# Kernel optimization log

Hardware: AMD Instinct MI355X
Metric: run time of the kernel (lower is better)

## Reference

```python
import jax, jax.numpy as jnp
import numpy as np

N, D, O, V, E, C = 100000, 128, 128, 3, 400000, 2

def setup_inputs() -> dict:
    key = jax.random.key(0)
    ks = jax.random.split(key, 32)
    s = 0.05
    inp = {
        'features': jax.random.normal(ks[0], (N, D), jnp.float32),
        'edge_index': jax.random.randint(ks[1], (V, 2, E), 0, N, jnp.int32),
        'edge_weight': jax.random.uniform(ks[2], (V, E), jnp.float32),
        # per-view RelationAggregator (single relation each)
        'rel_w': jax.random.normal(ks[3], (V, D, O)) * s,
        'rel_b': jnp.zeros((V, O)),
        'gate_w': jax.random.normal(ks[4], (V, O, O)) * s,
        'gate_b': jnp.zeros((V, O)),
        # LabelAwareAttention
        'la_w1': jax.random.normal(ks[5], (C, D, D // 2)) * s,
        'la_b1': jnp.zeros((C, D // 2)),
        'la_w2': jax.random.normal(ks[6], (C, D // 2)) * s,
        'la_b2': jnp.zeros((C,)),
        'pred_w': jax.random.normal(ks[7], (D, C)) * s,
        'pred_b': jnp.zeros((C,)),
        'att_bias': jnp.float32(0.1),
        # ViewLevelAttention
        'view_pref': jax.random.normal(ks[8], (V, O)),
        'va_w1': jax.random.normal(ks[9], (O, O // 2)) * s,
        'va_b1': jnp.zeros((O // 2,)),
        'va_w2': jax.random.normal(ks[10], (O // 2,)) * s,
        'va_b2': jnp.float32(0.0),
        # linear heads
        'ft_w': jax.random.normal(ks[11], (D, O)) * s,
        'ft_b': jnp.zeros((O,)),
        'sl_w': jax.random.normal(ks[12], (D, O)) * s,
        'sl_b': jnp.zeros((O,)),
        'fus_w': jax.random.normal(ks[13], (2 * O, O)) * s,
        'fus_b': jnp.zeros((O,)),
        'ln_g': jnp.ones((O,)),
        'ln_beta': jnp.zeros((O,)),
    }
    return inp


def _aggregate_view(features, ei, ew, w, b, gw, gb):
    # gather -> linear -> edge weight -> scatter-add (fused segment_sum)
    msg = (features[ei[0]] @ w + b) * ew[:, None]          # [E, O]
    agg = jax.ops.segment_sum(msg, ei[1], num_segments=N)  # [N, O]
    # relation_weight_net: softmax over 1 relation == 1.0 (identity)
    gate = jax.nn.sigmoid(agg @ gw + gb)
    return gate * agg


def reference(features, edge_index, edge_weight, rel_w, rel_b, gate_w, gate_b,
              la_w1, la_b1, la_w2, la_b2, pred_w, pred_b, att_bias,
              view_pref, va_w1, va_b1, va_w2, va_b2,
              ft_w, ft_b, sl_w, sl_b, fus_w, fus_b, ln_g, ln_beta):
    # --- label-aware attention ---
    class_probs = jax.nn.softmax(features @ pred_w + pred_b, axis=-1)        # [N, C]
    h = jax.nn.relu(jnp.einsum('nd,cdk->nck', features, la_w1) + la_b1)      # [N, C, D/2]
    scores = jax.nn.sigmoid(jnp.einsum('nck,ck->nc', h, la_w2) + la_b2)      # [N, C]
    node_att = jnp.sum(scores * class_probs, axis=-1) + att_bias             # [N]

    # --- per-view relation aggregation ---
    views = jax.vmap(_aggregate_view, in_axes=(None, 0, 0, 0, 0, 0, 0))(
        features, edge_index, edge_weight, rel_w, rel_b, gate_w, gate_b)     # [V, N, O]

    # --- view-level attention ---
    pe = views * view_pref[:, None, :]                                       # [V, N, O]
    vh = jax.nn.relu(jnp.einsum('vno,ok->vnk', pe, va_w1) + va_b1)           # [V, N, O/2]
    vscore = jnp.einsum('vnk,k->vn', vh, va_w2) + va_b2                      # [V, N]
    v_att = jax.nn.softmax(vscore, axis=0)                                   # over views
    combined = jnp.sum(views * v_att[..., None], axis=0)                     # [N, O]

    # --- fusion (dropout in eval mode == identity) ---
    self_out = features @ sl_w + sl_b
    transformed = features @ ft_w + ft_b
    weighted = combined * node_att[:, None]
    fused = jax.nn.relu(jnp.concatenate([self_out, weighted], axis=-1) @ fus_w + fus_b)
    out = fused + transformed

    mu = jnp.mean(out, axis=-1, keepdims=True)
    var = jnp.mean(jnp.square(out - mu), axis=-1, keepdims=True)
    out = (out - mu) / jnp.sqrt(var + 1e-5) * ln_g + ln_beta
    return out, class_probs
```

## Files before the change

### kernel.cpp

```cpp
#include <hip/hip_runtime.h>

#define N_ 100000
#define D_ 128
#define O_ 128
#define V_ 3
#define E_ 400000
#define NB_SCAN 98
#define EGRID 1563
#define MB 32
#define NBLK (N_ / MB)
#define LDA 136

#define PRE_CVT  6250
#define PRE_PREW (PRE_CVT + 64)
#define PRE_PREP (PRE_PREW + 617)
#define PRE_TOT  (PRE_PREP + 3 * EGRID)

typedef unsigned short u16;
typedef __attribute__((ext_vector_type(8))) short bf16x8;
typedef __attribute__((ext_vector_type(4))) float f32x4;

#define MFMA16x16x32 __builtin_amdgcn_mfma_f32_16x16x32_bf16

#define P_RELB  0
#define P_GATEB 384
#define P_VP    768
#define P_VAB1  1152
#define P_VAW2  1216
#define P_VAB2  1280
#define P_LAB1  1281
#define P_LAW2  1409
#define P_LAB2  1537
#define P_PREDB 1539
#define P_ATTB  1541
#define P_FTB   1542
#define P_LNG   1670
#define P_LNB   1798
#define P_PREDW 1926
#define P_TOTAL 2182

__device__ __forceinline__ float b2f(u16 u) {
    union { float f; unsigned int i; } x; x.i = ((unsigned int)u) << 16; return x.f;
}
__device__ __forceinline__ float blo(unsigned int u) {
    union { float f; unsigned int i; } x; x.i = u << 16; return x.f;
}
__device__ __forceinline__ float bhi(unsigned int u) {
    union { float f; unsigned int i; } x; x.i = u & 0xffff0000u; return x.f;
}
__device__ __forceinline__ u16 f2b(float f) {
    union { float f; unsigned int i; } x; x.f = f;
    unsigned int r = x.i + 0x7FFFu + ((x.i >> 16) & 1u);
    return (u16)(r >> 16);
}

template<int F32> __device__ __forceinline__ float LD(const void* p, size_t i) {
    if (F32) return ((const float*)p)[i];
    return b2f(((const u16*)p)[i]);
}

__global__ void k_detect(const u16* __restrict__ feat, int* __restrict__ flag) {
    int t = threadIdx.x;
    u16 a = feat[2 * t], b = feat[2 * t + 128];
    int zeros = (a == 0 ? 1 : 0) + (b == 0 ? 1 : 0);
    float va = b2f(a), vb = b2f(b);
    int bad = (!(va > -128.f && va < 128.f) ? 1 : 0) +
              (!(vb > -128.f && vb < 128.f) ? 1 : 0);
    #pragma unroll
    for (int s = 1; s <= 32; s <<= 1) {
        bad += __shfl_xor(bad, s);
        zeros += __shfl_xor(zeros, s);
    }
    if (t == 0) flag[0] = (bad >= 16 || zeros >= 64) ? 1 : 0;
}

__device__ __forceinline__ void cvt_body_f32(int b, const void* feat,
                                             u16* __restrict__ featB) {
    size_t idx = (size_t)b * 256 + threadIdx.x;
    const float4* fp = (const float4*)feat;
    float4 a = fp[idx * 2], c = fp[idx * 2 + 1];
    uint4 u;
    u.x = (unsigned)f2b(a.x) | ((unsigned)f2b(a.y) << 16);
    u.y = (unsigned)f2b(a.z) | ((unsigned)f2b(a.w) << 16);
    u.z = (unsigned)f2b(c.x) | ((unsigned)f2b(c.y) << 16);
    u.w = (unsigned)f2b(c.z) | ((unsigned)f2b(c.w) << 16);
    ((uint4*)featB)[idx] = u;
}

template<int F32>
__device__ __forceinline__ void prew_body(int b, const void* sl_w, const void* sl_b,
                                          const void* fus_w, const void* fus_b,
                                          u16* __restrict__ W1T, float* __restrict__ b1) {
    int gid = b * 256 + threadIdx.x;
    int d = gid >> 7, o = gid & 127;
    float acc = 0.f;
    for (int k = 0; k < 128; ++k)
        acc += LD<F32>(sl_w, d * 128 + k) * LD<F32>(fus_w, k * 128 + o);
    W1T[o * 128 + d] = f2b(acc);
    if (gid < 128) {
        float accb = 0.f;
        for (int k = 0; k < 128; ++k)
            accb += LD<F32>(sl_b, k) * LD<F32>(fus_w, k * 128 + gid);
        b1[gid] = accb + LD<F32>(fus_b, gid);
    }
}

template<int F32>
__device__ __forceinline__ void prep_body(int b,
        const void* rel_w, const void* gate_w, const void* va_w1, const void* fus_w,
        const void* ft_w, const void* la_w1,
        const void* rel_b, const void* gate_b, const void* vpref,
        const void* va_b1, const void* va_w2, const void* va_b2,
        const void* la_b1, const void* la_w2, const void* la_b2,
        const void* pred_b, const void* att_bias, const void* ft_b,
        const void* ln_g, const void* ln_beta, const void* pred_w,
        u16* __restrict__ relT, u16* __restrict__ gateT, u16* __restrict__ vaT,
        u16* __restrict__ fus2T, u16* __restrict__ ftT, u16* __restrict__ laT,
        float* __restrict__ P) {
    int id = b * 256 + threadIdx.x;
    if (id < 49152) {
        int v = id >> 14, r = id & 16383, o = r >> 7, d = r & 127;
        relT[id] = f2b(LD<F32>(rel_w, (size_t)v * 16384 + d * 128 + o));
    } else if (id < 98304) {
        int t = id - 49152, v = t >> 14, r = t & 16383, o = r >> 7, d = r & 127;
        gateT[t] = f2b(LD<F32>(gate_w, (size_t)v * 16384 + d * 128 + o));
    } else if (id < 106496) {
        int t = id - 98304, n = t >> 7, k = t & 127;
        vaT[t] = f2b(LD<F32>(va_w1, k * 64 + n));
    } else if (id < 122880) {
        int t = id - 106496, n = t >> 7, k = t & 127;
        fus2T[t] = f2b(LD<F32>(fus_w, (128 + k) * 128 + n));
    } else if (id < 139264) {
        int t = id - 122880, o = t >> 7, d = t & 127;
        ftT[t] = f2b(LD<F32>(ft_w, d * 128 + o));
    } else if (id < 155648) {
        int t = id - 139264, n = t >> 7, d = t & 127;
        int c = n >> 6, j = n & 63;
        laT[t] = f2b(LD<F32>(la_w1, c * 8192 + d * 64 + j));
    } else if (id < 155648 + P_TOTAL) {
        int t = id - 155648;
        float val;
        if      (t < P_GATEB) val = LD<F32>(rel_b, t);
        else if (t < P_VP)    val = LD<F32>(gate_b, t - P_GATEB);
        else if (t < P_VAB1)  val = LD<F32>(vpref, t - P_VP);
        else if (t < P_VAW2)  val = LD<F32>(va_b1, t - P_VAB1);
        else if (t < P_VAB2)  val = LD<F32>(va_w2, t - P_VAW2);
        else if (t < P_LAB1)  val = LD<F32>(va_b2, 0);
        else if (t < P_LAW2)  val = LD<F32>(la_b1, t - P_LAB1);
        else if (t < P_LAB2)  val = LD<F32>(la_w2, t - P_LAW2);
        else if (t < P_PREDB) val = LD<F32>(la_b2, t - P_LAB2);
        else if (t < P_ATTB)  val = LD<F32>(pred_b, t - P_PREDB);
        else if (t < P_FTB)   val = LD<F32>(att_bias, 0);
        else if (t < P_LNG)   val = LD<F32>(ft_b, t - P_FTB);
        else if (t < P_LNB)   val = LD<F32>(ln_g, t - P_LNG);
        else if (t < P_PREDW) val = LD<F32>(ln_beta, t - P_LNB);
        else                  val = LD<F32>(pred_w, t - P_PREDW);
        P[t] = val;
    }
}

__global__ __launch_bounds__(256) void k_preC(const int* __restrict__ flag,
        const void* feat, u16* __restrict__ featB,
        const void* sl_w, const void* sl_b, const void* fus_w, const void* fus_b,
        u16* __restrict__ W1T, float* __restrict__ b1,
        const void* rel_w, const void* gate_w, const void* va_w1,
        const void* ft_w, const void* la_w1,
        const void* rel_b, const void* gate_b, const void* vpref,
        const void* va_b1, const void* va_w2, const void* va_b2,
        const void* la_b1, const void* la_w2, const void* la_b2,
        const void* pred_b, const void* att_bias, const void* ft_b,
        const void* ln_g, const void* ln_beta, const void* pred_w,
        u16* __restrict__ relT, u16* __restrict__ gateT, u16* __restrict__ vaT,
        u16* __restrict__ fus2T, u16* __restrict__ ftT, u16* __restrict__ laT,
        float* __restrict__ P,
        const int* __restrict__ ei, int* __restrict__ cur3) {
    int b = blockIdx.x;
    if (b < PRE_CVT) {
        if (flag[0]) cvt_body_f32(b, feat, featB);
    } else if (b < PRE_PREW) {
        if (flag[0]) prew_body<1>(b - PRE_CVT, sl_w, sl_b, fus_w, fus_b, W1T, b1);
        else         prew_body<0>(b - PRE_CVT, sl_w, sl_b, fus_w, fus_b, W1T, b1);
    } else if (b < PRE_PREP) {
        if (flag[0]) prep_body<1>(b - PRE_PREW, rel_w, gate_w, va_w1, fus_w, ft_w, la_w1,
                                  rel_b, gate_b, vpref, va_b1, va_w2, va_b2,
                                  la_b1, la_w2, la_b2, pred_b, att_bias, ft_b,
                                  ln_g, ln_beta, pred_w, relT, gateT, vaT, fus2T, ftT, laT, P);
        else         prep_body<0>(b - PRE_PREW, rel_w, gate_w, va_w1, fus_w, ft_w, la_w1,
                                  rel_b, gate_b, vpref, va_b1, va_w2, va_b2,
                                  la_b1, la_w2, la_b2, pred_b, att_bias, ft_b,
                                  ln_g, ln_beta, pred_w, relT, gateT, vaT, fus2T, ftT, laT, P);
    } else {
        int b2 = b - PRE_PREP;
        int v = b2 / EGRID;
        int e = (b2 % EGRID) * 256 + threadIdx.x;
        if (e < E_) atomicAdd(&cur3[v * N_ + ei[(size_t)v * 2 * E_ + E_ + e]], 1);
    }
}

__global__ __launch_bounds__(256) void k_scan_bsum(const int* __restrict__ cur3,
                                                   int* __restrict__ bsum) {
    __shared__ int red[256];
    const int v = blockIdx.x / NB_SCAN, b = blockIdx.x % NB_SCAN, tid = threadIdx.x;
    const int base = b * 1024;
    const int* counts = cur3 + v * N_;
    int s = 0;
    for (int i = tid; i < 1024; i += 256) {
        int idx = base + i;
        s += (idx < N_) ? counts[idx] : 0;
    }
    red[tid] = s;
    __syncthreads();
    for (int st = 128; st >= 1; st >>= 1) {
        if (tid < st) red[tid] += red[tid + st];
        __syncthreads();
    }
    if (tid == 0) bsum[v * 128 + b] = red[0];
}

__global__ __launch_bounds__(256) void k_scan_write(int* __restrict__ cur3,
                                                    const int* __restrict__ bsum,
                                                    int* __restrict__ offs3) {
    __shared__ int lsum[256];
    __shared__ int bs_s[128];
    const int v = blockIdx.x / NB_SCAN, b = blockIdx.x % NB_SCAN, tid = threadIdx.x;
    const int base = b * 1024;
    int* counts = cur3 + v * N_;
    int* offs   = offs3 + v * N_;
    if (tid < 128) bs_s[tid] = (tid < b) ? bsum[v * 128 + tid] : 0;
    int c[4]; int s = 0;
    #pragma unroll
    for (int k = 0; k < 4; ++k) {
        int idx = base + tid * 4 + k;
        c[k] = (idx < N_) ? counts[idx] : 0;
        s += c[k];
    }
    lsum[tid] = s;
    __syncthreads();
    for (int st = 1; st < 256; st <<= 1) {
        int t = (tid >= st) ? lsum[tid - st] : 0;
        __syncthreads();
        lsum[tid] += t;
        __syncthreads();
    }
    for (int st = 64; st >= 1; st >>= 1) {
        if (tid < st) bs_s[tid] += bs_s[tid + st];
        __syncthreads();
    }
    int off = bs_s[0] + lsum[tid] - s;
    #pragma unroll
    for (int k = 0; k < 4; ++k) {
        int idx = base + tid * 4 + k;
        if (idx < N_) { offs[idx] = off; counts[idx] = off; }
        off += c[k];
    }
}

template<int F32>
__device__ __forceinline__ void place_body(const int* __restrict__ ei, const void* ew_all,
                                           int* __restrict__ cur3, int2* __restrict__ srcw3) {
    int v = blockIdx.x / EGRID;
    int e = (blockIdx.x % EGRID) * 256 + threadIdx.x;
    if (e < E_) {
        int dst = ei[(size_t)v * 2 * E_ + E_ + e];
        int src = ei[(size_t)v * 2 * E_ + e];
        float w = LD<F32>(ew_all, (size_t)v * E_ + e);
        int pos = atomicAdd(&cur3[v * N_ + dst], 1);
        int2 sw; sw.x = src; sw.y = __float_as_int(w);
        srcw3[(size_t)v * E_ + pos] = sw;
    }
}
__global__ __launch_bounds__(256) void k_place(const int* __restrict__ flag,
                                               const int* __restrict__ ei, const void* ew,
                                               int* __restrict__ cur3, int2* __restrict__ srcw3) {
    if (flag[0]) place_body<1>(ei, ew, cur3, srcw3);
    else         place_body<0>(ei, ew, cur3, srcw3);
}

__global__ __launch_bounds__(768, 6) void k_fused(const int* __restrict__ flag,
        const void* feat, const u16* __restrict__ featB_,
        const int2* __restrict__ srcw3,
        const int* __restrict__ offs3, const int* __restrict__ ends3,
        const u16* __restrict__ relT, const u16* __restrict__ gateT,
        const u16* __restrict__ vaT, const u16* __restrict__ W1T,
        const u16* __restrict__ fus2T, const u16* __restrict__ ftT,
        const u16* __restrict__ laT,
        const float* __restrict__ b1, const float* __restrict__ P,
        void* __restrict__ d_out) {
    const int f32 = flag[0];
    const u16* __restrict__ fb = f32 ? featB_ : (const u16*)feat;

    __shared__ __align__(16) u16 xA[MB * LDA];
    __shared__ __align__(16) u16 zbuf[3][MB * LDA];
    __shared__ __align__(16) float Fbuf[MB * 128];
    __shared__ float vp3_s[3][128];
    __shared__ float redL[4][MB];
    __shared__ float redv[3][4][MB];
    __shared__ float wsn3[3][MB];
    __shared__ float aw_s[MB][3];
    __shared__ float natt_s[MB];
    __shared__ float lg_s[MB][2];
    __shared__ float mrs_s[MB][2];
    __shared__ float vab1_s[64], vaw2_s[64];
    __shared__ float predw_s[256];
    __shared__ float b1_s[128], ftb_s[128], lng_s[128], lnb_s[128];

    const int tid = threadIdx.x;
    const int g   = tid >> 8;
    const int t256 = tid & 255;
    const int wid = t256 >> 6;
    const int L = t256 & 63, q = L >> 4, i = L & 15;
    const int nb = wid * 32;
    const int nodebase = blockIdx.x * MB;
    const int nl = t256 >> 5, l32 = t256 & 31, o4 = l32 * 4;
    const int gsub = t256 >> 4, l16 = tid & 15, o8 = l16 * 8;
    const f32x4 zz = {0.f, 0.f, 0.f, 0.f};

    auto ldf = [&](const u16* B, int row, int k0) -> bf16x8 {
        return *(const bf16x8*)&B[row * LDA + k0];
    };
    auto ldg = [&](const u16* B, int row, int k0) -> bf16x8 {
        return *(const bf16x8*)&B[row * 128 + k0];
    };
    auto gemm32 = [&](const u16* A, const u16* Bg, f32x4 acc[2][2]) {
        #pragma unroll
        for (int kk = 0; kk < 4; ++kk) {
            int k0 = q * 8 + kk * 32;
            bf16x8 a0 = ldf(A, i, k0);
            bf16x8 a1 = ldf(A, i + 16, k0);
            bf16x8 bb0 = ldg(Bg, nb + i, k0);
            bf16x8 bb1 = ldg(Bg, nb + 16 + i, k0);
            acc[0][0] = MFMA16x16x32(a0, bb0, acc[0][0], 0, 0, 0);
            acc[0][1] = MFMA16x16x32(a0, bb1, acc[0][1], 0, 0, 0);
            acc[1][0] = MFMA16x16x32(a1, bb0, acc[1][0], 0, 0, 0);
            acc[1][1] = MFMA16x16x32(a1, bb1, acc[1][1], 0, 0, 0);
        }
    };
    auto gather = [&]() {
        const int* offs = offs3 + g * N_;
        const int* ends = ends3 + g * N_;
        const int2* srcw = srcw3 + (size_t)g * E_;
        #pragma unroll
        for (int rep = 0; rep < 2; ++rep) {
            const int m = gsub + rep * 16;
            const int node = nodebase + m;
            float z0 = 0.f, z1 = 0.f, z2 = 0.f, z3 = 0.f;
            float z4 = 0.f, z5 = 0.f, z6 = 0.f, z7 = 0.f, ws = 0.f;
            int j = offs[node], jend = ends[node];
            while (j < jend) {
                int r = jend - j;
                int2 e0 = srcw[j];
                int2 e1, e2, e3;
                e1.x = 0; e1.y = 0; e2.x = 0; e2.y = 0; e3.x = 0; e3.y = 0;
                if (r > 1) e1 = srcw[j + 1];
                if (r > 2) e2 = srcw[j + 2];
                if (r > 3) e3 = srcw[j + 3];
                uint4 x0, x1, x2, x3;
                x1.x = x1.y = x1.z = x1.w = 0;
                x2.x = x2.y = x2.z = x2.w = 0;
                x3.x = x3.y = x3.z = x3.w = 0;
                x0 = *(const uint4*)&fb[(size_t)e0.x * 128 + o8];
                if (r > 1) x1 = *(const uint4*)&fb[(size_t)e1.x * 128 + o8];
                if (r > 2) x2 = *(const uint4*)&fb[(size_t)e2.x * 128 + o8];
                if (r > 3) x3 = *(const uint4*)&fb[(size_t)e3.x * 128 + o8];
                float w0 = __int_as_float(e0.y), w1 = __int_as_float(e1.y);
                float w2 = __int_as_float(e2.y), w3 = __int_as_float(e3.y);
                ws += w0 + w1 + w2 + w3;
                z0 += w0 * blo(x0.x) + w1 * blo(x1.x) + w2 * blo(x2.x) + w3 * blo(x3.x);
                z1 += w0 * bhi(x0.x) + w1 * bhi(x1.x) + w2 * bhi(x2.x) + w3 * bhi(x3.x);
                z2 += w0 * blo(x0.y) + w1 * blo(x1.y) + w2 * blo(x2.y) + w3 * blo(x3.y);
                z3 += w0 * bhi(x0.y) + w1 * bhi(x1.y) + w2 * bhi(x2.y) + w3 * bhi(x3.y);
                z4 += w0 * blo(x0.z) + w1 * blo(x1.z) + w2 * blo(x2.z) + w3 * blo(x3.z);
                z5 += w0 * bhi(x0.z) + w1 * bhi(x1.z) + w2 * bhi(x2.z) + w3 * bhi(x3.z);
                z6 += w0 * blo(x0.w) + w1 * blo(x1.w) + w2 * blo(x2.w) + w3 * blo(x3.w);
                z7 += w0 * bhi(x0.w) + w1 * bhi(x1.w) + w2 * bhi(x2.w) + w3 * bhi(x3.w);
                j += 4;
            }
            uint4 u;
            u.x = (unsigned)f2b(z0) | ((unsigned)f2b(z1) << 16);
            u.y = (unsigned)f2b(z2) | ((unsigned)f2b(z3) << 16);
            u.z = (unsigned)f2b(z4) | ((unsigned)f2b(z5) << 16);
            u.w = (unsigned)f2b(z6) | ((unsigned)f2b(z7) << 16);
            *(uint4*)&zbuf[g][m * LDA + o8] = u;
            if (l16 == 0) wsn3[g][m] = ws;
        }
    };

    if (tid < 512) {
        int m = tid >> 4, s = tid & 15;
        *(uint4*)&xA[m * LDA + s * 8] =
            *(const uint4*)&fb[(size_t)(nodebase + m) * 128 + s * 8];
    }
    if (tid < 64) { vab1_s[tid] = P[P_VAB1 + tid]; vaw2_s[tid] = P[P_VAW2 + tid]; }
    if (tid < 128) {
        b1_s[tid]  = b1[tid];
        ftb_s[tid] = P[P_FTB + tid];
        lng_s[tid] = P[P_LNG + tid];
        lnb_s[tid] = P[P_LNB + tid];
    }
    if (tid < 256) predw_s[tid] = P[P_PREDW + tid];
    if (tid >= 256 && tid < 640) {
        int t = tid - 256;
        vp3_s[t >> 7][t & 127] = P[P_VP + t];
    }
    gather();
    __syncthreads();

    f32x4 accA[2][2] = {{zz, zz}, {zz, zz}};
    gemm32(zbuf[g], relT + (size_t)g * 16384, accA);
    if (g == 0) {
        f32x4 accL[2][2] = {{zz, zz}, {zz, zz}};
        gemm32(xA, laT, accL);
        #pragma unroll
        for (int rep = 0; rep < 4; ++rep) {
            int m = rep * 8 + nl;
            float lg0 = 0.f, lg1 = 0.f;
            #pragma unroll
            for (int t = 0; t < 4; ++t) {
                float xv = b2f(xA[m * LDA + o4 + t]);
                lg0 += xv * predw_s[(o4 + t) * 2 + 0];
                lg1 += xv * predw_s[(o4 + t) * 2 + 1];
            }
            #pragma unroll
            for (int s = 1; s <= 16; s <<= 1) {
                lg0 += __shfl_xor(lg0, s);
                lg1 += __shfl_xor(lg1, s);
            }
            if (l32 == 0) { lg_s[m][0] = lg0; lg_s[m][1] = lg1; }
        }
        float la0 = P[P_LAB1 + nb + i],  la1 = P[P_LAB1 + nb + 16 + i];
        float lw0 = P[P_LAW2 + nb + i],  lw1 = P[P_LAW2 + nb + 16 + i];
        float partL[2][4];
        #pragma unroll
        for (int mt = 0; mt < 2; ++mt)
            #pragma unroll
            for (int r = 0; r < 4; ++r) {
                float h0 = fmaxf(accL[mt][0][r] + la0, 0.f);
                float h1 = fmaxf(accL[mt][1][r] + la1, 0.f);
                partL[mt][r] = h0 * lw0 + h1 * lw1;
            }
        #pragma unroll
        for (int s = 1; s <= 8; s <<= 1)
            #pragma unroll
            for (int mt = 0; mt < 2; ++mt)
                #pragma unroll
                for (int r = 0; r < 4; ++r)
                    partL[mt][r] += __shfl_xor(partL[mt][r], s);
        if (i == 0)
            #pragma unroll
            for (int mt = 0; mt < 2; ++mt)
                #pragma unroll
                for (int r = 0; r < 4; ++r)
                    redL[wid][mt * 16 + q * 4 + r] = partL[mt][r];
    }
    __syncthreads();

    {
        float rb0 = P[P_RELB + g * 128 + nb + i];
        float rb1 = P[P_RELB + g * 128 + nb + 16 + i];
        #pragma unroll
        for (int mt = 0; mt < 2; ++mt)
            #pragma unroll
            for (int nt = 0; nt < 2; ++nt) {
                float rb = nt ? rb1 : rb0;
                int col = nb + nt * 16 + i;
                #pragma unroll
                for (int r = 0; r < 4; ++r) {
                    int row = mt * 16 + q * 4 + r;
                    float a = accA[mt][nt][r] + wsn3[g][row] * rb;
                    accA[mt][nt][r] = a;
                    zbuf[g][row * LDA + col] = f2b(a);
                }
            }
    }
    if (tid < MB) {
        float c0 = redL[0][tid] + redL[1][tid] + P[P_LAB2 + 0];
        float c1 = redL[2][tid] + redL[3][tid] + P[P_LAB2 + 1];
        float s0 = 1.f / (1.f + __expf(-c0));
        float s1 = 1.f / (1.f + __expf(-c1));
        float l0 = lg_s[tid][0] + P[P_PREDB + 0];
        float l1 = lg_s[tid][1] + P[P_PREDB + 1];
        float mx = fmaxf(l0, l1);
        float e0 = __expf(l0 - mx), e1 = __expf(l1 - mx);
        float inv = 1.f / (e0 + e1);
        float p0 = e0 * inv, p1 = e1 * inv;
        natt_s[tid] = s0 * p0 + s1 * p1 + P[P_ATTB];
        int node = nodebase + tid;
        if (f32) {
            float* pr = (float*)d_out + (size_t)N_ * O_;
            pr[node * 2 + 0] = p0; pr[node * 2 + 1] = p1;
        } else {
            u16* pr = (u16*)d_out + (size_t)N_ * O_;
            pr[node * 2 + 0] = f2b(p0); pr[node * 2 + 1] = f2b(p1);
        }
    }
    __syncthreads();

    f32x4 acc2[2][2] = {{zz, zz}, {zz, zz}};
    gemm32(zbuf[g], gateT + (size_t)g * 16384, acc2);
    __syncthreads();

    {
        float gb0 = P[P_GATEB + g * 128 + nb + i];
        float gb1 = P[P_GATEB + g * 128 + nb + 16 + i];
        #pragma unroll
        for (int mt = 0; mt < 2; ++mt)
            #pragma unroll
            for (int nt = 0; nt < 2; ++nt) {
                float gb = nt ? gb1 : gb0;
                int col = nb + nt * 16 + i;
                #pragma unroll
                for (int r = 0; r < 4; ++r) {
                    int row = mt * 16 + q * 4 + r;
                    float gt = 1.f / (1.f + __expf(-(acc2[mt][nt][r] + gb)));
                    zbuf[g][row * LDA + col] = f2b(gt * accA[mt][nt][r]);
                }
            }
    }
    __syncthreads();

    {
        f32x4 accV[2] = {zz, zz};
        const int nbv = wid * 16, colv = nbv + i;
        #pragma unroll
        for (int kk = 0; kk < 4; ++kk) {
            int k0 = q * 8 + kk * 32;
            bf16x8 a0r = ldf(zbuf[g], i, k0);
            bf16x8 a1r = ldf(zbuf[g], i + 16, k0);
            bf16x8 a0, a1;
            #pragma unroll
            for (int e = 0; e < 8; ++e) {
                float vp = vp3_s[g][k0 + e];
                a0[e] = (short)f2b(b2f((u16)a0r[e]) * vp);
                a1[e] = (short)f2b(b2f((u16)a1r[e]) * vp);
            }
            bf16x8 bb = ldg(vaT, nbv + i, k0);
            accV[0] = MFMA16x16x32(a0, bb, accV[0], 0, 0, 0);
            accV[1] = MFMA16x16x32(a1, bb, accV[1], 0, 0, 0);
        }
        float part[2][4];
        #pragma unroll
        for (int mt = 0; mt < 2; ++mt)
            #pragma unroll
            for (int r = 0; r < 4; ++r) {
                float vh = fmaxf(accV[mt][r] + vab1_s[colv], 0.f);
                part[mt][r] = vh * vaw2_s[colv];
            }
        #pragma unroll
        for (int s = 1; s <= 8; s <<= 1)
            #pragma unroll
            for (int mt = 0; mt < 2; ++mt)
                #pragma unroll
                for (int r = 0; r < 4; ++r)
                    part[mt][r] += __shfl_xor(part[mt][r], s);
        if (i == 0)
            #pragma unroll
            for (int mt = 0; mt < 2; ++mt)
                #pragma unroll
                for (int r = 0; r < 4; ++r)
                    redv[g][wid][mt * 16 + q * 4 + r] = part[mt][r];
    }
    __syncthreads();

    if (tid < MB) {
        float sv[3];
        #pragma unroll
        for (int v = 0; v < 3; ++v)
            sv[v] = redv[v][0][tid] + redv[v][1][tid] +
                    redv[v][2][tid] + redv[v][3][tid] + P[P_VAB2];
        float mx = fmaxf(sv[0], fmaxf(sv[1], sv[2]));
        float e0 = __expf(sv[0] - mx), e1 = __expf(sv[1] - mx), e2 = __expf(sv[2] - mx);
        float inv = natt_s[tid] / (e0 + e1 + e2);
        aw_s[tid][0] = e0 * inv; aw_s[tid][1] = e1 * inv; aw_s[tid][2] = e2 * inv;
    }
    __syncthreads();

    for (int idx = tid; idx < MB * 128; idx += 768) {
        int row = idx >> 7, col = idx & 127;
        float w = aw_s[row][0] * b2f(zbuf[0][row * LDA + col]) +
                  aw_s[row][1] * b2f(zbuf[1][row * LDA + col]) +
                  aw_s[row][2] * b2f(zbuf[2][row * LDA + col]);
        zbuf[0][row * LDA + col] = f2b(w);
    }
    __syncthreads();

    float* F1 = (float*)&zbuf[1][0];
    f32x4 accG[2][2] = {{zz, zz}, {zz, zz}};
    if (g == 0) {
        gemm32(xA, W1T, accG);
        #pragma unroll
        for (int mt = 0; mt < 2; ++mt)
            #pragma unroll
            for (int nt = 0; nt < 2; ++nt)
                #pragma unroll
                for (int r = 0; r < 4; ++r)
                    F1[(mt * 16 + q * 4 + r) * 128 + nb + nt * 16 + i] = accG[mt][nt][r];
    } else if (g == 1) {
        gemm32(zbuf[0], fus2T, accG);
        #pragma unroll
        for (int mt = 0; mt < 2; ++mt)
            #pragma unroll
            for (int nt = 0; nt < 2; ++nt)
                #pragma unroll
                for (int r = 0; r < 4; ++r)
                    Fbuf[(mt * 16 + q * 4 + r) * 128 + nb + nt * 16 + i] = accG[mt][nt][r];
    } else {
        gemm32(xA, ftT, accG);
    }
    __syncthreads();

    float ov[2][2][4];
    if (g == 2) {
        float ps[2][4], pq[2][4];
        #pragma unroll
        for (int mt = 0; mt < 2; ++mt)
            #pragma unroll
            for (int r = 0; r < 4; ++r) { ps[mt][r] = 0.f; pq[mt][r] = 0.f; }
        #pragma unroll
        for (int mt = 0; mt < 2; ++mt)
            #pragma unroll
            for (int nt = 0; nt < 2; ++nt)
                #pragma unroll
                for (int r = 0; r < 4; ++r) {
                    int row = mt * 16 + q * 4 + r, col = nb + nt * 16 + i;
                    float o = fmaxf(F1[row * 128 + col] + Fbuf[row * 128 + col]
                                    + b1_s[col], 0.f)
                              + accG[mt][nt][r] + ftb_s[col];
                    ov[mt][nt][r] = o;
                    ps[mt][r] += o; pq[mt][r] += o * o;
                }
        #pragma unroll
        for (int s = 1; s <= 8; s <<= 1)
            #pragma unroll
            for (int mt = 0; mt < 2; ++mt)
                #pragma unroll
                for (int r = 0; r < 4; ++r) {
                    ps[mt][r] += __shfl_xor(ps[mt][r], s);
                    pq[mt][r] += __shfl_xor(pq[mt][r], s);
                }
        float* red2 = &redv[0][0][0];
        if (i == 0)
            #pragma unroll
            for (int mt = 0; mt < 2; ++mt)
                #pragma unroll
                for (int r = 0; r < 4; ++r) {
                    int row = mt * 16 + q * 4 + r;
                    red2[wid * 64 + row * 2 + 0] = ps[mt][r];
                    red2[wid * 64 + row * 2 + 1] = pq[mt][r];
                }
    }
    __syncthreads();

    if (tid < MB) {
        const float* red2 = &redv[0][0][0];
        float sm = red2[tid * 2] + red2[64 + tid * 2] +
                   red2[128 + tid * 2] + red2[192 + tid * 2];
        float sq = red2[tid * 2 + 1] + red2[64 + tid * 2 + 1] +
                   red2[128 + tid * 2 + 1] + red2[192 + tid * 2 + 1];
        float mu = sm * (1.f / 128.f);
        float var = sq * (1.f / 128.f) - mu * mu;
        mrs_s[tid][0] = mu; mrs_s[tid][1] = rsqrtf(var + 1e-5f);
    }
    __syncthreads();

    if (g == 2) {
        #pragma unroll
        for (int mt = 0; mt < 2; ++mt)
            #pragma unroll
            for (int nt = 0; nt < 2; ++nt)
                #pragma unroll
                for (int r = 0; r < 4; ++r) {
                    int row = mt * 16 + q * 4 + r, col = nb + nt * 16 + i;
                    float val = (ov[mt][nt][r] - mrs_s[row][0]) * mrs_s[row][1]
                                * lng_s[col] + lnb_s[col];
                    if (f32) Fbuf[row * 128 + col] = val;
                    else     ((u16*)Fbuf)[row * 128 + col] = f2b(val);
                }
    }
    __syncthreads();

    if (f32) {
        float* op = (float*)d_out + (size_t)nodebase * 128;
        for (int idx = tid; idx < 1024; idx += 768)
            ((float4*)op)[idx] = ((const float4*)Fbuf)[idx];
    } else {
        u16* op = (u16*)d_out + (size_t)nodebase * 128;
        if (tid < 512)
            ((uint4*)op)[tid] = ((const uint4*)Fbuf)[tid];
    }
}

extern "C" void kernel_launch(void* const* d_in, const int* in_sizes, int n_in,
                              void* d_out, int out_size, void* d_ws, size_t ws_size,
                              hipStream_t stream) {
    const void* feat     = d_in[0];
    const int*  ei       = (const int*)d_in[1];
    const void* ew       = d_in[2];
    const void* rel_w    = d_in[3];
    const void* rel_b    = d_in[4];
    const void* gate_w   = d_in[5];
    const void* gate_b   = d_in[6];
    const void* la_w1    = d_in[7];
    const void* la_b1    = d_in[8];
    const void* la_w2    = d_in[9];
    const void* la_b2    = d_in[10];
    const void* pred_w   = d_in[11];
    const void* pred_b   = d_in[12];
    const void* att_bias = d_in[13];
    const void* view_pref= d_in[14];
    const void* va_w1    = d_in[15];
    const void* va_b1    = d_in[16];
    const void* va_w2    = d_in[17];
    const void* va_b2    = d_in[18];
    const void* ft_w     = d_in[19];
    const void* ft_b     = d_in[20];
    const void* sl_w     = d_in[21];
    const void* sl_b     = d_in[22];
    const void* fus_w    = d_in[23];
    const void* fus_b    = d_in[24];
    const void* ln_g     = d_in[25];
    const void* ln_beta  = d_in[26];

    int*   flag  = (int*)d_ws;
    int*   offs3 = flag + 4;
    int*   cur3  = offs3 + 3 * N_;
    int2*  srcw3 = (int2*)(cur3 + 3 * N_);
    int*   bsum  = (int*)(srcw3 + 3 * E_);
    float* b1    = (float*)(bsum + 3 * 128);
    float* P     = b1 + 128;
    u16*   W1T   = (u16*)(P + 2304);
    u16*   relT  = W1T + 16384;
    u16*   gateT = relT + 3 * 16384;
    u16*   vaT   = gateT + 3 * 16384;
    u16*   fus2T = vaT + 8192;
    u16*   ftT   = fus2T + 16384;
    u16*   laT   = ftT + 16384;
    u16*   featB = laT + 16384;

    k_detect<<<1, 64, 0, stream>>>((const u16*)feat, flag);
    (void)hipMemsetAsync(cur3, 0, 3 * N_ * sizeof(int), stream);
    k_preC<<<PRE_TOT, 256, 0, stream>>>(flag, feat, featB,
                                        sl_w, sl_b, fus_w, fus_b, W1T, b1,
                                        rel_w, gate_w, va_w1, ft_w, la_w1,
                                        rel_b, gate_b, view_pref,
                                        va_b1, va_w2, va_b2,
                                        la_b1, la_w2, la_b2,
                                        pred_b, att_bias, ft_b, ln_g, ln_beta, pred_w,
                                        relT, gateT, vaT, fus2T, ftT, laT, P,
                                        ei, cur3);
    k_scan_bsum<<<3 * NB_SCAN, 256, 0, stream>>>(cur3, bsum);
    k_scan_write<<<3 * NB_SCAN, 256, 0, stream>>>(cur3, bsum, offs3);
    k_place<<<3 * EGRID, 256, 0, stream>>>(flag, ei, ew, cur3, srcw3);
    k_fused<<<NBLK, 768, 0, stream>>>(flag, feat, featB, srcw3, offs3, cur3,
                                      relT, gateT, vaT, W1T, fus2T, ftT, laT,
                                      b1, P, d_out);
}
```

Measured before the change: 544.2 us.

## Precompose relation and gate weights to run gate GEMM alongside aggregation GEMM

Precomputes rel_w@gate_w (and rel_b@gate_w) so the gate pre-activation is computed from the gathered input in the same MFMA pass as the aggregation, which removes a dependent GEMM and a barrier round-trip. It also folds view_pref into per-view va_w1 copies, which drops the per-element scaling in the view-attention GEMM. Shared memory is consolidated into one aliased buffer, and parameter staging into LDS is replaced by direct global loads. The layer-norm apply is fused into the output store. This adds a serial 128-length dot loop in the prep kernel, and the gate input now goes through bf16-rounded composed weights, so numerics shift slightly.

```diff
diff --git a/kernel.cpp b/kernel.cpp
--- a/kernel.cpp
+++ b/kernel.cpp
@@ -13,7 +13,7 @@
 
 #define PRE_CVT  6250
 #define PRE_PREW (PRE_CVT + 64)
-#define PRE_PREP (PRE_PREW + 617)
+#define PRE_PREP (PRE_PREW + 683)
 #define PRE_TOT  (PRE_PREP + 3 * EGRID)
 
 typedef unsigned short u16;
@@ -114,31 +114,28 @@
         const void* la_b1, const void* la_w2, const void* la_b2,
         const void* pred_b, const void* att_bias, const void* ft_b,
         const void* ln_g, const void* ln_beta, const void* pred_w,
-        u16* __restrict__ relT, u16* __restrict__ gateT, u16* __restrict__ vaT,
+        u16* __restrict__ relT, u16* __restrict__ rgT, u16* __restrict__ vaT3,
         u16* __restrict__ fus2T, u16* __restrict__ ftT, u16* __restrict__ laT,
-        float* __restrict__ P) {
+        float* __restrict__ P, float* __restrict__ rgb) {
     int id = b * 256 + threadIdx.x;
     if (id < 49152) {
         int v = id >> 14, r = id & 16383, o = r >> 7, d = r & 127;
         relT[id] = f2b(LD<F32>(rel_w, (size_t)v * 16384 + d * 128 + o));
-    } else if (id < 98304) {
-        int t = id - 49152, v = t >> 14, r = t & 16383, o = r >> 7, d = r & 127;
-        gateT[t] = f2b(LD<F32>(gate_w, (size_t)v * 16384 + d * 128 + o));
+    } else if (id < 73728) {
+        int t = id - 49152, v = t >> 13, r = t & 8191, n = r >> 7, k = r & 127;
+        vaT3[t] = f2b(LD<F32>(va_w1, k * 64 + n) * LD<F32>(vpref, v * 128 + k));
+    } else if (id < 90112) {
+        int t = id - 73728, n = t >> 7, k = t & 127;
+        fus2T[t] = f2b(LD<F32>(fus_w, (128 + k) * 128 + n));
     } else if (id < 106496) {
-        int t = id - 98304, n = t >> 7, k = t & 127;
-        vaT[t] = f2b(LD<F32>(va_w1, k * 64 + n));
+        int t = id - 90112, o = t >> 7, d = t & 127;
+        ftT[t] = f2b(LD<F32>(ft_w, d * 128 + o));
     } else if (id < 122880) {
-        int t = id - 106496, n = t >> 7, k = t & 127;
-        fus2T[t] = f2b(LD<F32>(fus_w, (128 + k) * 128 + n));
-    } else if (id < 139264) {
-        int t = id - 122880, o = t >> 7, d = t & 127;
-        ftT[t] = f2b(LD<F32>(ft_w, d * 128 + o));
-    } else if (id < 155648) {
-        int t = id - 139264, n = t >> 7, d = t & 127;
+        int t = id - 106496, n = t >> 7, d = t & 127;
         int c = n >> 6, j = n & 63;
         laT[t] = f2b(LD<F32>(la_w1, c * 8192 + d * 64 + j));
-    } else if (id < 155648 + P_TOTAL) {
-        int t = id - 155648;
+    } else if (id < 122880 + P_TOTAL) {
+        int t = id - 122880;
         float val;
         if      (t < P_GATEB) val = LD<F32>(rel_b, t);
         else if (t < P_VP)    val = LD<F32>(gate_b, t - P_GATEB);
@@ -156,6 +153,20 @@
         else if (t < P_PREDW) val = LD<F32>(ln_beta, t - P_LNB);
         else                  val = LD<F32>(pred_w, t - P_PREDW);
         P[t] = val;
+    } else if (id < 174214) {
+        int t = id - 125062, v = t >> 14, r = t & 16383, n = r >> 7, d = r & 127;
+        float acc = 0.f;
+        for (int o = 0; o < 128; ++o)
+            acc += LD<F32>(rel_w,  (size_t)v * 16384 + d * 128 + o) *
+                   LD<F32>(gate_w, (size_t)v * 16384 + o * 128 + n);
+        rgT[t] = f2b(acc);
+    } else if (id < 174598) {
+        int t = id - 174214, v = t >> 7, n = t & 127;
+        float acc = 0.f;
+        for (int o = 0; o < 128; ++o)
+            acc += LD<F32>(rel_b, v * 128 + o) *
+                   LD<F32>(gate_w, (size_t)v * 16384 + o * 128 + n);
+        rgb[t] = acc;
     }
 }
 
@@ -170,9 +181,9 @@
         const void* la_b1, const void* la_w2, const void* la_b2,
         const void* pred_b, const void* att_bias, const void* ft_b,
         const void* ln_g, const void* ln_beta, const void* pred_w,
-        u16* __restrict__ relT, u16* __restrict__ gateT, u16* __restrict__ vaT,
+        u16* __restrict__ relT, u16* __restrict__ rgT, u16* __restrict__ vaT3,
         u16* __restrict__ fus2T, u16* __restrict__ ftT, u16* __restrict__ laT,
-        float* __restrict__ P,
+        float* __restrict__ P, float* __restrict__ rgb,
         const int* __restrict__ ei, int* __restrict__ cur3) {
     int b = blockIdx.x;
     if (b < PRE_CVT) {
@@ -184,11 +195,11 @@
         if (flag[0]) prep_body<1>(b - PRE_PREW, rel_w, gate_w, va_w1, fus_w, ft_w, la_w1,
                                   rel_b, gate_b, vpref, va_b1, va_w2, va_b2,
                                   la_b1, la_w2, la_b2, pred_b, att_bias, ft_b,
-                                  ln_g, ln_beta, pred_w, relT, gateT, vaT, fus2T, ftT, laT, P);
+                                  ln_g, ln_beta, pred_w, relT, rgT, vaT3, fus2T, ftT, laT, P, rgb);
         else         prep_body<0>(b - PRE_PREW, rel_w, gate_w, va_w1, fus_w, ft_w, la_w1,
                                   rel_b, gate_b, vpref, va_b1, va_w2, va_b2,
                                   la_b1, la_w2, la_b2, pred_b, att_bias, ft_b,
-                                  ln_g, ln_beta, pred_w, relT, gateT, vaT, fus2T, ftT, laT, P);
+                                  ln_g, ln_beta, pred_w, relT, rgT, vaT3, fus2T, ftT, laT, P, rgb);
     } else {
         int b2 = b - PRE_PREP;
         int v = b2 / EGRID;
@@ -280,19 +291,17 @@
         const void* feat, const u16* __restrict__ featB_,
         const int2* __restrict__ srcw3,
         const int* __restrict__ offs3, const int* __restrict__ ends3,
-        const u16* __restrict__ relT, const u16* __restrict__ gateT,
-        const u16* __restrict__ vaT, const u16* __restrict__ W1T,
+        const u16* __restrict__ relT, const u16* __restrict__ rgT,
+        const u16* __restrict__ vaT3, const u16* __restrict__ W1T,
         const u16* __restrict__ fus2T, const u16* __restrict__ ftT,
         const u16* __restrict__ laT,
-        const float* __restrict__ b1, const float* __restrict__ P,
+        const float* __restrict__ b1, const float* __restrict__ rgb,
+        const float* __restrict__ P,
         void* __restrict__ d_out) {
     const int f32 = flag[0];
     const u16* __restrict__ fb = f32 ? featB_ : (const u16*)feat;
 
-    __shared__ __align__(16) u16 xA[MB * LDA];
-    __shared__ __align__(16) u16 zbuf[3][MB * LDA];
-    __shared__ __align__(16) float Fbuf[MB * 128];
-    __shared__ float vp3_s[3][128];
+    __shared__ __align__(16) u16 S[4 * MB * LDA];
     __shared__ float redL[4][MB];
     __shared__ float redv[3][4][MB];
     __shared__ float wsn3[3][MB];
@@ -300,9 +309,11 @@
     __shared__ float natt_s[MB];
     __shared__ float lg_s[MB][2];
     __shared__ float mrs_s[MB][2];
-    __shared__ float vab1_s[64], vaw2_s[64];
-    __shared__ float predw_s[256];
-    __shared__ float b1_s[128], ftb_s[128], lng_s[128], lnb_s[128];
+
+    u16* xA = S;
+    float* F1 = (float*)(S + 2 * MB * LDA);
+    float* F2 = (float*)S;
+    float* red2 = &redv[0][0][0];
 
     const int tid = threadIdx.x;
     const int g   = tid >> 8;
@@ -314,6 +325,7 @@
     const int nl = t256 >> 5, l32 = t256 & 31, o4 = l32 * 4;
     const int gsub = t256 >> 4, l16 = tid & 15, o8 = l16 * 8;
     const f32x4 zz = {0.f, 0.f, 0.f, 0.f};
+    u16* zc = S + (size_t)(1 + g) * MB * LDA;
 
     auto ldf = [&](const u16* B, int row, int k0) -> bf16x8 {
         return *(const bf16x8*)&B[row * LDA + k0];
@@ -333,6 +345,27 @@
             acc[0][1] = MFMA16x16x32(a0, bb1, acc[0][1], 0, 0, 0);
             acc[1][0] = MFMA16x16x32(a1, bb0, acc[1][0], 0, 0, 0);
             acc[1][1] = MFMA16x16x32(a1, bb1, acc[1][1], 0, 0, 0);
+        }
+    };
+    auto gemm32x2 = [&](const u16* A, const u16* B0g, const u16* B1g,
+                        f32x4 accA[2][2], f32x4 accB[2][2]) {
+        #pragma unroll
+        for (int kk = 0; kk < 4; ++kk) {
+            int k0 = q * 8 + kk * 32;
+            bf16x8 a0 = ldf(A, i, k0);
+            bf16x8 a1 = ldf(A, i + 16, k0);
+            bf16x8 p0 = ldg(B0g, nb + i, k0);
+            bf16x8 p1 = ldg(B0g, nb + 16 + i, k0);
+            bf16x8 r0 = ldg(B1g, nb + i, k0);
+            bf16x8 r1 = ldg(B1g, nb + 16 + i, k0);
+            accA[0][0] = MFMA16x16x32(a0, p0, accA[0][0], 0, 0, 0);
+            accA[0][1] = MFMA16x16x32(a0, p1, accA[0][1], 0, 0, 0);
+            accA[1][0] = MFMA16x16x32(a1, p0, accA[1][0], 0, 0, 0);
+            accA[1][1] = MFMA16x16x32(a1, p1, accA[1][1], 0, 0, 0);
+            accB[0][0] = MFMA16x16x32(a0, r0, accB[0][0], 0, 0, 0);
+            accB[0][1] = MFMA16x16x32(a0, r1, accB[0][1], 0, 0, 0);
+            accB[1][0] = MFMA16x16x32(a1, r0, accB[1][0], 0, 0, 0);
+            accB[1][1] = MFMA16x16x32(a1, r1, accB[1][1], 0, 0, 0);
         }
     };
     auto gather = [&]() {
@@ -380,7 +413,7 @@
             u.y = (unsigned)f2b(z2) | ((unsigned)f2b(z3) << 16);
             u.z = (unsigned)f2b(z4) | ((unsigned)f2b(z5) << 16);
             u.w = (unsigned)f2b(z6) | ((unsigned)f2b(z7) << 16);
-            *(uint4*)&zbuf[g][m * LDA + o8] = u;
+            *(uint4*)&zc[m * LDA + o8] = u;
             if (l16 == 0) wsn3[g][m] = ws;
         }
     };
@@ -390,26 +423,44 @@
         *(uint4*)&xA[m * LDA + s * 8] =
             *(const uint4*)&fb[(size_t)(nodebase + m) * 128 + s * 8];
     }
-    if (tid < 64) { vab1_s[tid] = P[P_VAB1 + tid]; vaw2_s[tid] = P[P_VAW2 + tid]; }
-    if (tid < 128) {
-        b1_s[tid]  = b1[tid];
-        ftb_s[tid] = P[P_FTB + tid];
-        lng_s[tid] = P[P_LNG + tid];
-        lnb_s[tid] = P[P_LNB + tid];
-    }
-    if (tid < 256) predw_s[tid] = P[P_PREDW + tid];
-    if (tid >= 256 && tid < 640) {
-        int t = tid - 256;
-        vp3_s[t >> 7][t & 127] = P[P_VP + t];
-    }
     gather();
     __syncthreads();
 
-    f32x4 accA[2][2] = {{zz, zz}, {zz, zz}};
-    gemm32(zbuf[g], relT + (size_t)g * 16384, accA);
-    if (g == 0) {
+    if (g == 1) {
         f32x4 accL[2][2] = {{zz, zz}, {zz, zz}};
         gemm32(xA, laT, accL);
+        float la0 = P[P_LAB1 + nb + i],  la1 = P[P_LAB1 + nb + 16 + i];
+        float lw0 = P[P_LAW2 + nb + i],  lw1 = P[P_LAW2 + nb + 16 + i];
+        float partL[2][4];
+        #pragma unroll
+        for (int mt = 0; mt < 2; ++mt)
+            #pragma unroll
+            for (int r = 0; r < 4; ++r) {
+                float h0 = fmaxf(accL[mt][0][r] + la0, 0.f);
+                float h1 = fmaxf(accL[mt][1][r] + la1, 0.f);
+                partL[mt][r] = h0 * lw0 + h1 * lw1;
+            }
+        #pragma unroll
+        for (int s = 1; s <= 8; s <<= 1)
+            #pragma unroll
+            for (int mt = 0; mt < 2; ++mt)
+                #pragma unroll
+                for (int r = 0; r < 4; ++r)
+                    partL[mt][r] += __shfl_xor(partL[mt][r], s);
+        if (i == 0)
+            #pragma unroll
+            for (int mt = 0; mt < 2; ++mt)
+                #pragma unroll
+                for (int r = 0; r < 4; ++r)
+                    redL[wid][mt * 16 + q * 4 + r] = partL[mt][r];
+    }
+    if (g == 2) {
+        float pw[8];
+        #pragma unroll
+        for (int t = 0; t < 4; ++t) {
+            pw[2 * t]     = P[P_PREDW + (o4 + t) * 2];
+            pw[2 * t + 1] = P[P_PREDW + (o4 + t) * 2 + 1];
+        }
         #pragma unroll
         for (int rep = 0; rep < 4; ++rep) {
             int m = rep * 8 + nl;
@@ -417,8 +468,8 @@
             #pragma unroll
             for (int t = 0; t < 4; ++t) {
                 float xv = b2f(xA[m * LDA + o4 + t]);
-                lg0 += xv * predw_s[(o4 + t) * 2 + 0];
-                lg1 += xv * predw_s[(o4 + t) * 2 + 1];
+                lg0 += xv * pw[2 * t];
+                lg1 += xv * pw[2 * t + 1];
             }
             #pragma unroll
             for (int s = 1; s <= 16; s <<= 1) {
@@ -427,48 +478,35 @@
             }
             if (l32 == 0) { lg_s[m][0] = lg0; lg_s[m][1] = lg1; }
         }
-        float la0 = P[P_LAB1 + nb + i],  la1 = P[P_LAB1 + nb + 16 + i];
-        float lw0 = P[P_LAW2 + nb + i],  lw1 = P[P_LAW2 + nb + 16 + i];
-        float partL[2][4];
-        #pragma unroll
-        for (int mt = 0; mt < 2; ++mt)
-            #pragma unroll
-            for (int r = 0; r < 4; ++r) {
-                float h0 = fmaxf(accL[mt][0][r] + la0, 0.f);
-                float h1 = fmaxf(accL[mt][1][r] + la1, 0.f);
-                partL[mt][r] = h0 * lw0 + h1 * lw1;
-            }
-        #pragma unroll
-        for (int s = 1; s <= 8; s <<= 1)
-            #pragma unroll
-            for (int mt = 0; mt < 2; ++mt)
-                #pragma unroll
-                for (int r = 0; r < 4; ++r)
-                    partL[mt][r] += __shfl_xor(partL[mt][r], s);
-        if (i == 0)
-            #pragma unroll
-            for (int mt = 0; mt < 2; ++mt)
-                #pragma unroll
-                for (int r = 0; r < 4; ++r)
-                    redL[wid][mt * 16 + q * 4 + r] = partL[mt][r];
-    }
+    }
+    f32x4 accA[2][2] = {{zz, zz}, {zz, zz}};
+    f32x4 accG[2][2] = {{zz, zz}, {zz, zz}};
+    gemm32x2(zc, relT + (size_t)g * 16384, rgT + (size_t)g * 16384, accA, accG);
     __syncthreads();
 
     {
         float rb0 = P[P_RELB + g * 128 + nb + i];
         float rb1 = P[P_RELB + g * 128 + nb + 16 + i];
+        float rg0 = rgb[g * 128 + nb + i];
+        float rg1 = rgb[g * 128 + nb + 16 + i];
+        float gb0 = P[P_GATEB + g * 128 + nb + i];
+        float gb1 = P[P_GATEB + g * 128 + nb + 16 + i];
         #pragma unroll
         for (int mt = 0; mt < 2; ++mt)
             #pragma unroll
             for (int nt = 0; nt < 2; ++nt) {
                 float rb = nt ? rb1 : rb0;
+                float rg = nt ? rg1 : rg0;
+                float gb = nt ? gb1 : gb0;
                 int col = nb + nt * 16 + i;
                 #pragma unroll
                 for (int r = 0; r < 4; ++r) {
                     int row = mt * 16 + q * 4 + r;
-                    float a = accA[mt][nt][r] + wsn3[g][row] * rb;
-                    accA[mt][nt][r] = a;
-                    zbuf[g][row * LDA + col] = f2b(a);
+                    float ws = wsn3[g][row];
+                    float agg = accA[mt][nt][r] + ws * rb;
+                    float gin = accG[mt][nt][r] + ws * rg + gb;
+                    float gt = 1.f / (1.f + __expf(-gin));
+                    zc[row * LDA + col] = f2b(gt * agg);
                 }
             }
     }
@@ -495,55 +533,27 @@
     }
     __syncthreads();
 
-    f32x4 acc2[2][2] = {{zz, zz}, {zz, zz}};
-    gemm32(zbuf[g], gateT + (size_t)g * 16384, acc2);
-    __syncthreads();
-
-    {
-        float gb0 = P[P_GATEB + g * 128 + nb + i];
-        float gb1 = P[P_GATEB + g * 128 + nb + 16 + i];
-        #pragma unroll
-        for (int mt = 0; mt < 2; ++mt)
-            #pragma unroll
-            for (int nt = 0; nt < 2; ++nt) {
-                float gb = nt ? gb1 : gb0;
-                int col = nb + nt * 16 + i;
-                #pragma unroll
-                for (int r = 0; r < 4; ++r) {
-                    int row = mt * 16 + q * 4 + r;
-                    float gt = 1.f / (1.f + __expf(-(acc2[mt][nt][r] + gb)));
-                    zbuf[g][row * LDA + col] = f2b(gt * accA[mt][nt][r]);
-                }
-            }
-    }
-    __syncthreads();
-
     {
         f32x4 accV[2] = {zz, zz};
         const int nbv = wid * 16, colv = nbv + i;
+        const u16* vaW = vaT3 + (size_t)g * 8192;
         #pragma unroll
         for (int kk = 0; kk < 4; ++kk) {
             int k0 = q * 8 + kk * 32;
-            bf16x8 a0r = ldf(zbuf[g], i, k0);
-            bf16x8 a1r = ldf(zbuf[g], i + 16, k0);
-            bf16x8 a0, a1;
-            #pragma unroll
-            for (int e = 0; e < 8; ++e) {
-                float vp = vp3_s[g][k0 + e];
-                a0[e] = (short)f2b(b2f((u16)a0r[e]) * vp);
-                a1[e] = (short)f2b(b2f((u16)a1r[e]) * vp);
-            }
-            bf16x8 bb = ldg(vaT, nbv + i, k0);
+            bf16x8 bb = ldg(vaW, nbv + i, k0);
+            bf16x8 a0 = ldf(zc, i, k0);
+            bf16x8 a1 = ldf(zc, i + 16, k0);
             accV[0] = MFMA16x16x32(a0, bb, accV[0], 0, 0, 0);
             accV[1] = MFMA16x16x32(a1, bb, accV[1], 0, 0, 0);
         }
+        float vb1v = P[P_VAB1 + colv], vw2v = P[P_VAW2 + colv];
         float part[2][4];
         #pragma unroll
         for (int mt = 0; mt < 2; ++mt)
             #pragma unroll
             for (int r = 0; r < 4; ++r) {
-                float vh = fmaxf(accV[mt][r] + vab1_s[colv], 0.f);
-                part[mt][r] = vh * vaw2_s[colv];
+                float vh = fmaxf(accV[mt][r] + vb1v, 0.f);
+                part[mt][r] = vh * vw2v;
             }
         #pragma unroll
         for (int s = 1; s <= 8; s <<= 1)
@@ -574,42 +584,50 @@
     }
     __syncthreads();
 
-    for (int idx = tid; idx < MB * 128; idx += 768) {
-        int row = idx >> 7, col = idx & 127;
-        float w = aw_s[row][0] * b2f(zbuf[0][row * LDA + col]) +
-                  aw_s[row][1] * b2f(zbuf[1][row * LDA + col]) +
-                  aw_s[row][2] * b2f(zbuf[2][row * LDA + col]);
-        zbuf[0][row * LDA + col] = f2b(w);
-    }
-    __syncthreads();
-
-    float* F1 = (float*)&zbuf[1][0];
-    f32x4 accG[2][2] = {{zz, zz}, {zz, zz}};
+    {
+        u16* z0p = S + MB * LDA;
+        u16* z1p = S + 2 * MB * LDA;
+        u16* z2p = S + 3 * MB * LDA;
+        for (int idx = tid; idx < MB * 128; idx += 768) {
+            int row = idx >> 7, col = idx & 127;
+            float w = aw_s[row][0] * b2f(z0p[row * LDA + col]) +
+                      aw_s[row][1] * b2f(z1p[row * LDA + col]) +
+                      aw_s[row][2] * b2f(z2p[row * LDA + col]);
+            z0p[row * LDA + col] = f2b(w);
+        }
+    }
+    __syncthreads();
+
+    f32x4 accF[2][2] = {{zz, zz}, {zz, zz}};
     if (g == 0) {
-        gemm32(xA, W1T, accG);
+        gemm32(xA, W1T, accF);
         #pragma unroll
         for (int mt = 0; mt < 2; ++mt)
             #pragma unroll
             for (int nt = 0; nt < 2; ++nt)
                 #pragma unroll
                 for (int r = 0; r < 4; ++r)
-                    F1[(mt * 16 + q * 4 + r) * 128 + nb + nt * 16 + i] = accG[mt][nt][r];
+                    F1[(mt * 16 + q * 4 + r) * 128 + nb + nt * 16 + i] = accF[mt][nt][r];
     } else if (g == 1) {
-        gemm32(zbuf[0], fus2T, accG);
+        gemm32(S + MB * LDA, fus2T, accF);
+    } else {
+        gemm32(xA, ftT, accF);
+    }
+    __syncthreads();
+    if (g == 1) {
         #pragma unroll
         for (int mt = 0; mt < 2; ++mt)
             #pragma unroll
             for (int nt = 0; nt < 2; ++nt)
                 #pragma unroll
                 for (int r = 0; r < 4; ++r)
-                    Fbuf[(mt * 16 + q * 4 + r) * 128 + nb + nt * 16 + i] = accG[mt][nt][r];
-    } else {
-        gemm32(xA, ftT, accG);
-    }
-    __syncthreads();
-
-    float ov[2][2][4];
+                    F2[(mt * 16 + q * 4 + r) * 128 + nb + nt * 16 + i] = accF[mt][nt][r];
+    }
+    __syncthreads();
+
     if (g == 2) {
+        float b1v0 = b1[nb + i], b1v1 = b1[nb + 16 + i];
+        float fb0 = P[P_FTB + nb + i], fb1 = P[P_FTB + nb + 16 + i];
         float ps[2][4], pq[2][4];
         #pragma unroll
         for (int mt = 0; mt < 2; ++mt)
@@ -618,16 +636,18 @@
         #pragma unroll
         for (int mt = 0; mt < 2; ++mt)
             #pragma unroll
-            for (int nt = 0; nt < 2; ++nt)
+            for (int nt = 0; nt < 2; ++nt) {
+                int col = nb + nt * 16 + i;
+                float bv = nt ? b1v1 : b1v0;
+                float fv = nt ? fb1 : fb0;
                 #pragma unroll
                 for (int r = 0; r < 4; ++r) {
-                    int row = mt * 16 + q * 4 + r, col = nb + nt * 16 + i;
-                    float o = fmaxf(F1[row * 128 + col] + Fbuf[row * 128 + col]
-                                    + b1_s[col], 0.f)
-                              + accG[mt][nt][r] + ftb_s[col];
-                    ov[mt][nt][r] = o;
+                    int rc = (mt * 16 + q * 4 + r) * 128 + col;
+                    float o = fmaxf(F1[rc] + F2[rc] + bv, 0.f) + accF[mt][nt][r] + fv;
+                    F1[rc] = o;
                     ps[mt][r] += o; pq[mt][r] += o * o;
                 }
+            }
         #pragma unroll
         for (int s = 1; s <= 8; s <<= 1)
             #pragma unroll
@@ -637,55 +657,45 @@
                     ps[mt][r] += __shfl_xor(ps[mt][r], s);
                     pq[mt][r] += __shfl_xor(pq[mt][r], s);
                 }
-        float* red2 = &redv[0][0][0];
         if (i == 0)
             #pragma unroll
             for (int mt = 0; mt < 2; ++mt)
                 #pragma unroll
                 for (int r = 0; r < 4; ++r) {
                     int row = mt * 16 + q * 4 + r;
-                    red2[wid * 64 + row * 2 + 0] = ps[mt][r];
-                    red2[wid * 64 + row * 2 + 1] = pq[mt][r];
+                    red2[(wid * MB + row) * 2 + 0] = ps[mt][r];
+                    red2[(wid * MB + row) * 2 + 1] = pq[mt][r];
                 }
     }
     __syncthreads();
 
     if (tid < MB) {
-        const float* red2 = &redv[0][0][0];
-        float sm = red2[tid * 2] + red2[64 + tid * 2] +
-                   red2[128 + tid * 2] + red2[192 + tid * 2];
-        float sq = red2[tid * 2 + 1] + red2[64 + tid * 2 + 1] +
-                   red2[128 + tid * 2 + 1] + red2[192 + tid * 2 + 1];
+        float sm = red2[tid * 2]            + red2[(MB + tid) * 2] +
+                   red2[(2 * MB + tid) * 2] + red2[(3 * MB + tid) * 2];
+        float sq = red2[tid * 2 + 1]            + red2[(MB + tid) * 2 + 1] +
+                   red2[(2 * MB + tid) * 2 + 1] + red2[(3 * MB + tid) * 2 + 1];
         float mu = sm * (1.f / 128.f);
         float var = sq * (1.f / 128.f) - mu * mu;
         mrs_s[tid][0] = mu; mrs_s[tid][1] = rsqrtf(var + 1e-5f);
     }
     __syncthreads();
 
-    if (g == 2) {
-        #pragma unroll
-        for (int mt = 0; mt < 2; ++mt)
-            #pragma unroll
-            for (int nt = 0; nt < 2; ++nt)
-                #pragma unroll
-                for (int r = 0; r < 4; ++r) {
-                    int row = mt * 16 + q * 4 + r, col = nb + nt * 16 + i;
-                    float val = (ov[mt][nt][r] - mrs_s[row][0]) * mrs_s[row][1]
-                                * lng_s[col] + lnb_s[col];
-                    if (f32) Fbuf[row * 128 + col] = val;
-                    else     ((u16*)Fbuf)[row * 128 + col] = f2b(val);
-                }
-    }
-    __syncthreads();
-
     if (f32) {
         float* op = (float*)d_out + (size_t)nodebase * 128;
-        for (int idx = tid; idx < 1024; idx += 768)
-            ((float4*)op)[idx] = ((const float4*)Fbuf)[idx];
+        for (int idx = tid; idx < MB * 128; idx += 768) {
+            int row = idx >> 7, col = idx & 127;
+            op[idx] = (F1[idx] - mrs_s[row][0]) * mrs_s[row][1]
+                      * P[P_LNG + col] + P[P_LNB + col];
+        }
     } else {
-        u16* op = (u16*)d_out + (size_t)nodebase * 128;
-        if (tid < 512)
-            ((uint4*)op)[tid] = ((const uint4*)Fbuf)[tid];
+        unsigned* op = (unsigned*)d_out + (size_t)nodebase * 64;
+        for (int idx = tid; idx < MB * 64; idx += 768) {
+            int row = idx >> 6, c2 = (idx & 63) * 2;
+            float m0 = mrs_s[row][0], r0 = mrs_s[row][1];
+            float v0 = (F1[row * 128 + c2]     - m0) * r0 * P[P_LNG + c2]     + P[P_LNB + c2];
+            float v1 = (F1[row * 128 + c2 + 1] - m0) * r0 * P[P_LNG + c2 + 1] + P[P_LNB + c2 + 1];
+            op[idx] = (unsigned)f2b(v0) | ((unsigned)f2b(v1) << 16);
+        }
     }
 }
 
@@ -727,11 +737,12 @@
     int*   bsum  = (int*)(srcw3 + 3 * E_);
     float* b1    = (float*)(bsum + 3 * 128);
     float* P     = b1 + 128;
-    u16*   W1T   = (u16*)(P + 2304);
+    float* rgb   = P + 2304;
+    u16*   W1T   = (u16*)(rgb + 384);
     u16*   relT  = W1T + 16384;
-    u16*   gateT = relT + 3 * 16384;
-    u16*   vaT   = gateT + 3 * 16384;
-    u16*   fus2T = vaT + 8192;
+    u16*   rgT   = relT + 3 * 16384;
+    u16*   vaT3  = rgT + 3 * 16384;
+    u16*   fus2T = vaT3 + 3 * 8192;
     u16*   ftT   = fus2T + 16384;
     u16*   laT   = ftT + 16384;
     u16*   featB = laT + 16384;
@@ -745,12 +756,12 @@
                                         va_b1, va_w2, va_b2,
                                         la_b1, la_w2, la_b2,
                                         pred_b, att_bias, ft_b, ln_g, ln_beta, pred_w,
-                                        relT, gateT, vaT, fus2T, ftT, laT, P,
+                                        relT, rgT, vaT3, fus2T, ftT, laT, P, rgb,
                                         ei, cur3);
     k_scan_bsum<<<3 * NB_SCAN, 256, 0, stream>>>(cur3, bsum);
     k_scan_write<<<3 * NB_SCAN, 256, 0, stream>>>(cur3, bsum, offs3);
     k_place<<<3 * EGRID, 256, 0, stream>>>(flag, ei, ew, cur3, srcw3);
     k_fused<<<NBLK, 768, 0, stream>>>(flag, feat, featB, srcw3, offs3, cur3,
-                                      relT, gateT, vaT, W1T, fus2T, ftT, laT,
-                                      b1, P, d_out);
-}
+                                      relT, rgT, vaT3, W1T, fus2T, ftT, laT,
+                                      b1, rgb, P, d_out);
+}
```

After: 517.5 us. 1.05x faster.
